# Performance work log

Measured on AMD Instinct MI355X. Metric: run time of the kernel, lower is better.

Reference implementation:

```python
import jax, jax.numpy as jnp
import numpy as np

N_NODES = 50000
N_EDGES = 800000
NUM_EMBS = 50000
EMB = 128
HID = 256
OUT = 128
NUM_GRAPHS = 256


def gcn_conv(x, W, b, src, dst, n):
    # PyG GCNConv: add self-loops, sym-normalize, aggregate, linear.
    h = x @ W  # [n, d_out]
    ones = jnp.ones((src.shape[0],), dtype=x.dtype)
    deg = jax.ops.segment_sum(ones, dst, num_segments=n) + 1.0  # +1 self-loop
    dinv = jax.lax.rsqrt(deg)  # deg^{-1/2}
    norm = dinv[src] * dinv[dst]  # per-edge norm
    msg = h[src] * norm[:, None]  # gather + scale  [E, d_out]
    agg = jax.ops.segment_sum(msg, dst, num_segments=n)
    agg = agg + h * (dinv * dinv)[:, None]  # self-loop term 1/deg[i]
    return agg + b


def scatter_mean(x, seg, num_segments):
    s = jax.ops.segment_sum(x, seg, num_segments=num_segments)
    cnt = jax.ops.segment_sum(jnp.ones((x.shape[0],), x.dtype), seg, num_segments=num_segments)
    return s / jnp.maximum(cnt, 1.0)[:, None]


def setup_inputs() -> dict:
    key = jax.random.key(0)
    ks = jax.random.split(key, 12)
    node_ids = jax.random.randint(ks[0], (N_NODES,), 0, NUM_EMBS)
    edge_index = jax.random.randint(ks[1], (2, N_EDGES), 0, N_NODES)
    batch = jnp.sort(jax.random.randint(ks[2], (N_NODES,), 0, NUM_GRAPHS))
    s = 0.05
    embed = jax.random.normal(ks[3], (NUM_EMBS, EMB), jnp.float32) * s
    W_in = jax.random.normal(ks[4], (EMB, HID), jnp.float32) * s
    b_in = jnp.zeros((HID,), jnp.float32)
    W_h1 = jax.random.normal(ks[5], (HID, HID), jnp.float32) * s
    b_h1 = jnp.zeros((HID,), jnp.float32)
    W_h2 = jax.random.normal(ks[6], (HID, HID), jnp.float32) * s
    b_h2 = jnp.zeros((HID,), jnp.float32)
    W_out = jax.random.normal(ks[7], (HID, OUT), jnp.float32) * s
    b_out = jnp.zeros((OUT,), jnp.float32)
    return {"node_ids": node_ids, "edge_index": edge_index, "batch": batch,
            "embed": embed, "W_in": W_in, "b_in": b_in,
            "W_h1": W_h1, "b_h1": b_h1, "W_h2": W_h2, "b_h2": b_h2,
            "W_out": W_out, "b_out": b_out}


def reference(node_ids, edge_index, batch, embed, W_in, b_in, W_h1, b_h1, W_h2, b_h2, W_out, b_out):
    src, dst = edge_index[0], edge_index[1]
    n = node_ids.shape[0]
    x = embed[node_ids]  # [N, EMB]
    x = gcn_conv(x, W_in, b_in, src, dst, n)
    x = jax.nn.relu(x)  # dropout = identity (eval mode)
    for W, b in ((W_h1, b_h1), (W_h2, b_h2)):
        x = gcn_conv(x, W, b, src, dst, n) + x  # residual
        x = jax.nn.relu(x)
    x = gcn_conv(x, W_out, b_out, src, dst, n)
    return scatter_mean(x, batch, NUM_GRAPHS)  # [NUM_GRAPHS, OUT]
```

## Files before the change

### kernel.cpp

```cpp
#include <hip/hip_runtime.h>
#include <hip/hip_bf16.h>
#include <hip/hip_fp8.h>

#define N_NODES 50000
#define N_EDGES 800000
#define EMB_D 128
#define HID_D 256
#define OUT_D 128
#define NGRAPH 256

#define SCAN_B ((N_NODES + 256) / 256)
#define MAX_CSR (N_EDGES + 7 * N_NODES)

typedef __attribute__((ext_vector_type(8))) short short8;
typedef __attribute__((ext_vector_type(4))) float floatx4;
typedef __attribute__((ext_vector_type(4))) unsigned short ushortx4;
typedef __attribute__((ext_vector_type(8))) unsigned short ushortx8;
typedef __attribute__((ext_vector_type(4))) unsigned char ucharx4;
typedef __attribute__((ext_vector_type(8))) unsigned char ucharx8;

__device__ inline unsigned short f2b(float f) {
    __hip_bfloat16 h = __float2bfloat16(f);
    return *reinterpret_cast<unsigned short*>(&h);
}

__device__ inline float b2f(unsigned short u) {
    union { unsigned int i; float f; } c;
    c.i = ((unsigned int)u) << 16;
    return c.f;
}

__device__ inline unsigned char f2f8(float f) {
    __hip_fp8_e4m3 v(f);
    return (unsigned char)v.__x;
}

__device__ inline float h2f(unsigned short u) { return b2f(u); }
__device__ inline float h2f(unsigned char u) {
    __hip_fp8_e4m3 v; v.__x = (__hip_fp8_storage_t)u;
    return (float)v;
}

template<int D, typename HT> struct HVec;
template<> struct HVec<128, unsigned short> { using T = ushortx4; };
template<> struct HVec<256, unsigned short> { using T = ushortx8; };
template<> struct HVec<128, unsigned char>  { using T = ucharx4;  };
template<> struct HVec<256, unsigned char>  { using T = ucharx8;  };

__global__ void rank_kernel(const int* __restrict__ dst, int* __restrict__ deg4,
                            int* __restrict__ pos) {
    int e = blockIdx.x * blockDim.x + threadIdx.x;
    if (e >= N_EDGES) return;
    pos[e] = atomicAdd(&deg4[(size_t)(e & 3) * N_NODES + dst[e]], 1);
}

__global__ void scan_a(const int* __restrict__ deg4, int* __restrict__ degt,
                       int* __restrict__ degp, int* __restrict__ sb4,
                       int* __restrict__ bsum, float* __restrict__ dinv) {
    __shared__ int red[256];
    int t = threadIdx.x;
    int i = blockIdx.x * 256 + t;
    int pad = 0;
    if (i < N_NODES) {
        int d0 = deg4[i];
        int d1 = deg4[(size_t)N_NODES + i];
        int d2 = deg4[(size_t)2 * N_NODES + i];
        int d3 = deg4[(size_t)3 * N_NODES + i];
        int tot = d0 + d1 + d2 + d3;
        degt[i] = tot;
        pad = (tot + 7) & ~7;
        degp[i] = pad;
        dinv[i] = rsqrtf((float)tot + 1.0f);
        sb4[i] = 0;
        sb4[(size_t)N_NODES + i] = d0;
        sb4[(size_t)2 * N_NODES + i] = d0 + d1;
        sb4[(size_t)3 * N_NODES + i] = d0 + d1 + d2;
    }
    red[t] = pad;
    __syncthreads();
    for (int off = 128; off > 0; off >>= 1) {
        if (t < off) red[t] += red[t + off];
        __syncthreads();
    }
    if (t == 0) bsum[blockIdx.x] = red[0];
}

__global__ void scan_b(const int* __restrict__ bsum, int* __restrict__ boff,
                       const int* __restrict__ batch, int* __restrict__ bstart) {
    int t = threadIdx.x;
    {
        int lo = 0, hi = N_NODES;
        while (lo < hi) {
            int mid = (lo + hi) >> 1;
            if (batch[mid] < t) lo = mid + 1;
            else hi = mid;
        }
        bstart[t] = lo;
        if (t == 0) bstart[NGRAPH] = N_NODES;
    }
    __shared__ int s[256];
    s[t] = (t < SCAN_B) ? bsum[t] : 0;
    __syncthreads();
    for (int off = 1; off < 256; off <<= 1) {
        int v = (t >= off) ? s[t - off] : 0;
        __syncthreads();
        s[t] += v;
        __syncthreads();
    }
    if (t < SCAN_B) boff[t] = (t == 0) ? 0 : s[t - 1];
}

__global__ void scan_c(const int* __restrict__ degp, const int* __restrict__ degt,
                       const int* __restrict__ boff, int* __restrict__ row_start,
                       unsigned int* __restrict__ csr) {
    __shared__ int s[256];
    int t = threadIdx.x;
    int i = blockIdx.x * 256 + t;
    int v = (i < N_NODES) ? degp[i] : 0;
    s[t] = v;
    __syncthreads();
    for (int off = 1; off < 256; off <<= 1) {
        int x = (t >= off) ? s[t - off] : 0;
        __syncthreads();
        s[t] += x;
        __syncthreads();
    }
    int excl = s[t] - v;
    int rs = boff[blockIdx.x] + excl;
    if (i <= N_NODES) row_start[i] = rs;
    if (i < N_NODES) {
        int e_true = rs + degt[i];
        int e_end  = rs + degp[i];
        for (int k = e_true; k < e_end; ++k) csr[k] = 0u;
    }
}

__global__ void scatter_kernel(const int* __restrict__ src, const int* __restrict__ dst,
                               const int* __restrict__ pos, const int* __restrict__ row_start,
                               const int* __restrict__ sb4, const float* __restrict__ dinv,
                               unsigned int* __restrict__ csr) {
    int e = blockIdx.x * blockDim.x + threadIdx.x;
    if (e >= N_EDGES) return;
    int s = src[e], d = dst[e];
    int slot = row_start[d] + sb4[(size_t)(e & 3) * N_NODES + d] + pos[e];
    csr[slot] = ((unsigned int)f2b(dinv[s] * dinv[d]) << 16) | (unsigned int)s;
}

template<int K, int D>
__device__ inline void wsplit_one(int idx, const float* __restrict__ W,
                                  short* __restrict__ wb) {
    int j = idx & 7;
    int l = (idx >> 3) & 63;
    int rest = idx >> 9;
    int kb = rest % (K / 32);
    int t = rest / (K / 32);
    int k = kb * 32 + (l >> 4) * 8 + j;
    int ncol = t * 16 + (l & 15);
    wb[idx] = (short)f2b(W[(size_t)k * D + ncol]);
}

__global__ void prep_kernel(const int* __restrict__ ids, const float* __restrict__ embed,
                            unsigned char* __restrict__ E8,
                            const float* __restrict__ W_in, const float* __restrict__ W_h1,
                            const float* __restrict__ W_h2, const float* __restrict__ W_out,
                            short* __restrict__ wb_in, short* __restrict__ wb_h1,
                            short* __restrict__ wb_h2, short* __restrict__ wb_out) {
    int idx = blockIdx.x * blockDim.x + threadIdx.x;
    constexpr int GV = N_NODES * (EMB_D / 4);
    if (idx < GV) {
        const int V = EMB_D / 4;
        int row = idx / V, c = idx % V;
        float4 v = ((const float4*)embed)[(size_t)ids[row] * V + c];
        ucharx4 u;
        u[0] = f2f8(v.x); u[1] = f2f8(v.y); u[2] = f2f8(v.z); u[3] = f2f8(v.w);
        ((ucharx4*)E8)[idx] = u;
        return;
    }
    int j = idx - GV;
    constexpr int S1 = EMB_D * HID_D;
    constexpr int S2 = S1 + HID_D * HID_D;
    constexpr int S3 = S2 + HID_D * HID_D;
    constexpr int S4 = S3 + HID_D * OUT_D;
    if (j < S1)      wsplit_one<EMB_D, HID_D>(j,      W_in,  wb_in);
    else if (j < S2) wsplit_one<HID_D, HID_D>(j - S1, W_h1,  wb_h1);
    else if (j < S3) wsplit_one<HID_D, HID_D>(j - S2, W_h2,  wb_h2);
    else if (j < S4) wsplit_one<HID_D, OUT_D>(j - S3, W_out, wb_out);
}

template<int D, typename HT, bool HASB, bool RES, bool RELU, bool BOUT>
__global__ __launch_bounds__(256) void agg_node(
        const int* __restrict__ row_start, const unsigned int* __restrict__ csr,
        const float* __restrict__ dinv, const HT* __restrict__ H,
        const float* __restrict__ b, float* __restrict__ OUTF,
        unsigned short* __restrict__ Pb) {
    constexpr int V2 = D / 32;
    using UV = typename HVec<D, HT>::T;
    using RV = typename HVec<D, unsigned short>::T;
    int wave = threadIdx.x >> 6, lane = threadIdx.x & 63;
    int i = blockIdx.x * 4 + wave;
    if (i >= N_NODES) return;
    int h = lane >> 5, q = lane & 31;
    const int off = q * V2;
    const HT* __restrict__ Hoff = H + off;
    float acc0[V2], acc1[V2];
#pragma unroll
    for (int v = 0; v < V2; ++v) { acc0[v] = 0.f; acc1[v] = 0.f; }
    int e0 = row_start[i], e1 = row_start[i + 1];
    if (e0 < e1) {
        unsigned int sn0 = csr[e0 + h];
        unsigned int sn1 = csr[e0 + 2 + h];
        unsigned int sn2 = csr[e0 + 4 + h];
        unsigned int sn3 = csr[e0 + 6 + h];
        int e = e0 + 8;
        for (;;) {
            UV u0 = *(const UV*)(Hoff + (size_t)(sn0 & 0xFFFFu) * D);
            UV u1 = *(const UV*)(Hoff + (size_t)(sn1 & 0xFFFFu) * D);
            UV u2 = *(const UV*)(Hoff + (size_t)(sn2 & 0xFFFFu) * D);
            UV u3 = *(const UV*)(Hoff + (size_t)(sn3 & 0xFFFFu) * D);
            float n0 = b2f((unsigned short)(sn0 >> 16));
            float n1 = b2f((unsigned short)(sn1 >> 16));
            float n2 = b2f((unsigned short)(sn2 >> 16));
            float n3 = b2f((unsigned short)(sn3 >> 16));
            bool more = (e < e1);
            unsigned int t0, t1, t2, t3;
            if (more) {
                t0 = csr[e + h];
                t1 = csr[e + 2 + h];
                t2 = csr[e + 4 + h];
                t3 = csr[e + 6 + h];
            }
#pragma unroll
            for (int v = 0; v < V2; ++v) acc0[v] = fmaf(h2f(u0[v]), n0, acc0[v]);
#pragma unroll
            for (int v = 0; v < V2; ++v) acc1[v] = fmaf(h2f(u1[v]), n1, acc1[v]);
#pragma unroll
            for (int v = 0; v < V2; ++v) acc0[v] = fmaf(h2f(u2[v]), n2, acc0[v]);
#pragma unroll
            for (int v = 0; v < V2; ++v) acc1[v] = fmaf(h2f(u3[v]), n3, acc1[v]);
            if (!more) break;
            sn0 = t0; sn1 = t1; sn2 = t2; sn3 = t3;
            e += 8;
        }
    }
#pragma unroll
    for (int v = 0; v < V2; ++v) {
        float s = acc0[v] + acc1[v];
        acc0[v] = s + __shfl_xor(s, 32);
    }
    if (h == 0) {
        float di = dinv[i];
        float d2 = di * di;
        UV us = *(const UV*)(Hoff + (size_t)i * D);
        RV rb;
        if (RES) rb = *(const RV*)(Pb + (size_t)i * D + off);
        RV ob;
#pragma unroll
        for (int v = 0; v < V2; ++v) {
            float val = acc0[v];
            val = fmaf(h2f(us[v]), d2, val);
            if (HASB) val += b[off + v];
            if (RES)  val += b2f(rb[v]);
            if (RELU) val = fmaxf(val, 0.f);
            if (BOUT) ob[v] = f2b(val);
            else      OUTF[(size_t)i * D + off + v] = val;
        }
        if (BOUT) *(RV*)(Pb + (size_t)i * D + off) = ob;
    }
}

template<int K, int D, bool BIAS, bool RELU, int OMODE>
__global__ __launch_bounds__(256) void gemm_mfma(
        const unsigned short* __restrict__ A_g, const short* __restrict__ Wb,
        const float* __restrict__ b, void* __restrict__ OutB, int n) {
    constexpr int LDK = K + 8;
    constexpr int NT = D / 64;
    constexpr int KB = K / 32;
    __shared__ __align__(16) short Ab[64 * LDK];

    int row0 = blockIdx.x * 64;
    constexpr int NF8 = 64 * (K / 8);
    for (int idx = threadIdx.x; idx < NF8; idx += 256) {
        int r = idx / (K / 8), c8 = idx % (K / 8);
        ushortx8 vh = {0, 0, 0, 0, 0, 0, 0, 0};
        if (row0 + r < n)
            vh = *(const ushortx8*)(A_g + (size_t)(row0 + r) * K + c8 * 8);
        *(ushortx8*)&Ab[r * LDK + c8 * 8] = vh;
    }
    __syncthreads();

    int wave = threadIdx.x >> 6, lane = threadIdx.x & 63;
    int quad = lane >> 4, lane15 = lane & 15;

    floatx4 acc[4][NT];
#pragma unroll
    for (int mt = 0; mt < 4; ++mt)
#pragma unroll
        for (int nt = 0; nt < NT; ++nt)
            acc[mt][nt] = (floatx4){0.f, 0.f, 0.f, 0.f};

#pragma unroll
    for (int kb = 0; kb < KB; ++kb) {
        short8 ah[4];
#pragma unroll
        for (int mt = 0; mt < 4; ++mt) {
            int addr = (mt * 16 + lane15) * LDK + kb * 32 + quad * 8;
            ah[mt] = *(const short8*)&Ab[addr];
        }
        short8 bh[NT];
#pragma unroll
        for (int nt = 0; nt < NT; ++nt) {
            int t = wave * NT + nt;
            size_t fb = ((size_t)(t * KB + kb) * 64 + lane) * 8;
            bh[nt] = *(const short8*)&Wb[fb];
        }
#pragma unroll
        for (int mt = 0; mt < 4; ++mt)
#pragma unroll
            for (int nt = 0; nt < NT; ++nt)
                acc[mt][nt] = __builtin_amdgcn_mfma_f32_16x16x32_bf16(ah[mt], bh[nt], acc[mt][nt], 0, 0, 0);
    }

#pragma unroll
    for (int mt = 0; mt < 4; ++mt) {
#pragma unroll
        for (int nt = 0; nt < NT; ++nt) {
            int col = wave * (NT * 16) + nt * 16 + lane15;
            float bj = BIAS ? b[col] : 0.f;
#pragma unroll
            for (int reg = 0; reg < 4; ++reg) {
                int row = row0 + mt * 16 + quad * 4 + reg;
                if (row < n) {
                    float v = acc[mt][nt][reg] + bj;
                    if (RELU) v = fmaxf(v, 0.f);
                    if (OMODE == 2) ((unsigned char*)OutB)[(size_t)row * D + col] = f2f8(v);
                    else            ((unsigned short*)OutB)[(size_t)row * D + col] = f2b(v);
                }
            }
        }
    }
}

__global__ void graph_mean(const int* __restrict__ bstart, const float* __restrict__ X,
                           float* __restrict__ out) {
    int g = blockIdx.x;
    int r0 = bstart[g], r1 = bstart[g + 1];
    int col = threadIdx.x & 127, rr = threadIdx.x >> 7;
    float acc = 0.f;
    for (int r = r0 + rr; r < r1; r += 2)
        acc += X[(size_t)r * OUT_D + col];
    __shared__ float sh[128];
    if (rr == 1) sh[col] = acc;
    __syncthreads();
    if (rr == 0) {
        float tot = acc + sh[col];
        int c = r1 - r0;
        out[(size_t)g * OUT_D + col] = tot / (float)(c > 0 ? c : 1);
    }
}

extern "C" void kernel_launch(void* const* d_in, const int* in_sizes, int n_in,
                              void* d_out, int out_size, void* d_ws, size_t ws_size,
                              hipStream_t stream) {
    const int* node_ids = (const int*)d_in[0];
    const int* edge_index = (const int*)d_in[1];
    const int* batch = (const int*)d_in[2];
    const float* embed = (const float*)d_in[3];
    const float* W_in  = (const float*)d_in[4];
    const float* b_in  = (const float*)d_in[5];
    const float* W_h1  = (const float*)d_in[6];
    const float* b_h1  = (const float*)d_in[7];
    const float* W_h2  = (const float*)d_in[8];
    const float* b_h2  = (const float*)d_in[9];
    const float* W_out = (const float*)d_in[10];
    const float* b_out = (const float*)d_in[11];
    float* out = (float*)d_out;

    const int* src = edge_index;
    const int* dst = edge_index + N_EDGES;

    char* w = (char*)d_ws;
    size_t o = 0;
    auto alloc = [&](size_t bytes) -> void* {
        void* p = w + o;
        o = (o + bytes + 255) & ~(size_t)255;
        return p;
    };
    int*   deg4     = (int*)alloc((size_t)4 * N_NODES * sizeof(int));
    int*   sb4      = (int*)alloc((size_t)4 * N_NODES * sizeof(int));
    int*   degt     = (int*)alloc((size_t)N_NODES * sizeof(int));
    int*   degp     = (int*)alloc((size_t)N_NODES * sizeof(int));
    int*   pos      = (int*)alloc((size_t)N_EDGES * sizeof(int));
    float* dinv     = (float*)alloc((size_t)N_NODES * sizeof(float));
    int*   bstart   = (int*)alloc((size_t)(NGRAPH + 1) * sizeof(int));
    int*   row_start= (int*)alloc((size_t)(N_NODES + 1) * sizeof(int));
    int*   bsum     = (int*)alloc((size_t)SCAN_B * sizeof(int));
    int*   boff     = (int*)alloc((size_t)SCAN_B * sizeof(int));
    unsigned int* csr = (unsigned int*)alloc((size_t)MAX_CSR * sizeof(unsigned int));
    unsigned short* Xb  = (unsigned short*)alloc((size_t)N_NODES * HID_D * sizeof(short));
    unsigned char*  E8  = (unsigned char*)alloc((size_t)N_NODES * EMB_D);
    unsigned char*  H8  = (unsigned char*)alloc((size_t)N_NODES * HID_D);
    unsigned short* A1b = (unsigned short*)alloc((size_t)N_NODES * 128 * sizeof(short));
    float* A1       = (float*)alloc((size_t)N_NODES * 128 * sizeof(float));
    short* Wb_in    = (short*)alloc((size_t)EMB_D * HID_D * sizeof(short));
    short* Wb_h1    = (short*)alloc((size_t)HID_D * HID_D * sizeof(short));
    short* Wb_h2    = (short*)alloc((size_t)HID_D * HID_D * sizeof(short));
    short* Wb_out   = (short*)alloc((size_t)HID_D * OUT_D * sizeof(short));
    unsigned char* H8_4 = H8;
    (void)ws_size;

    hipMemsetAsync(deg4, 0, (size_t)4 * N_NODES * sizeof(int), stream);

    rank_kernel<<<(N_EDGES + 255) / 256, 256, 0, stream>>>(dst, deg4, pos);
    scan_a<<<SCAN_B, 256, 0, stream>>>(deg4, degt, degp, sb4, bsum, dinv);
    scan_b<<<1, 256, 0, stream>>>(bsum, boff, batch, bstart);
    scan_c<<<SCAN_B, 256, 0, stream>>>(degp, degt, boff, row_start, csr);
    scatter_kernel<<<(N_EDGES + 255) / 256, 256, 0, stream>>>(src, dst, pos, row_start,
                                                              sb4, dinv, csr);

    constexpr int GV = N_NODES * (EMB_D / 4);
    prep_kernel<<<(GV + 196608 + 255) / 256, 256, 0, stream>>>(
        node_ids, embed, E8, W_in, W_h1, W_h2, W_out, Wb_in, Wb_h1, Wb_h2, Wb_out);

    const int gemm_grid = (N_NODES + 63) / 64;
    const int agg_grid = (N_NODES + 3) / 4;

    agg_node<128, unsigned char, false, false, false, true><<<agg_grid, 256, 0, stream>>>(
        row_start, csr, dinv, E8, nullptr, nullptr, A1b);
    gemm_mfma<128, 256, true, true, 0><<<gemm_grid, 256, 0, stream>>>(
        A1b, Wb_in, b_in, Xb, N_NODES);

    gemm_mfma<256, 256, false, false, 2><<<gemm_grid, 256, 0, stream>>>(
        Xb, Wb_h1, nullptr, H8, N_NODES);
    agg_node<256, unsigned char, true, true, true, true><<<agg_grid, 256, 0, stream>>>(
        row_start, csr, dinv, H8, b_h1, nullptr, Xb);

    gemm_mfma<256, 256, false, false, 2><<<gemm_grid, 256, 0, stream>>>(
        Xb, Wb_h2, nullptr, H8, N_NODES);
    agg_node<256, unsigned char, true, true, true, true><<<agg_grid, 256, 0, stream>>>(
        row_start, csr, dinv, H8, b_h2, nullptr, Xb);

    gemm_mfma<256, 128, false, false, 2><<<gemm_grid, 256, 0, stream>>>(
        Xb, Wb_out, nullptr, H8_4, N_NODES);
    agg_node<128, unsigned char, true, false, false, false><<<agg_grid, 256, 0, stream>>>(
        row_start, csr, dinv, H8_4, b_out, A1, nullptr);

    graph_mean<<<NGRAPH, 256, 0, stream>>>(bstart, A1, out);
}
```

Before: 395.7 us.

## Widen aggregation gathers to 8-element vectors and store final layer in bf16

The node aggregation kernel now has each lane gather 8 contiguous features. For D=128 this splits the wave into four 16-lane edge groups instead of two, so four edges are in flight per gather slot instead of two. The partial sums are then reduced across groups with a shuffle tree. The final aggregation writes bf16 instead of fp32, and the graph-mean kernel reads packed bf16 pairs with four row streams, which halves output traffic. Wider loads should improve memory efficiency, at the cost of extra shuffles and reduced precision on the last layer's output.

```diff
diff --git a/kernel.cpp b/kernel.cpp
--- a/kernel.cpp
+++ b/kernel.cpp
@@ -41,11 +41,9 @@
     return (float)v;
 }
 
-template<int D, typename HT> struct HVec;
-template<> struct HVec<128, unsigned short> { using T = ushortx4; };
-template<> struct HVec<256, unsigned short> { using T = ushortx8; };
-template<> struct HVec<128, unsigned char>  { using T = ucharx4;  };
-template<> struct HVec<256, unsigned char>  { using T = ucharx8;  };
+template<typename HT> struct UV8;
+template<> struct UV8<unsigned short> { using T = ushortx8; };
+template<> struct UV8<unsigned char>  { using T = ucharx8;  };
 
 __global__ void rank_kernel(const int* __restrict__ dst, int* __restrict__ deg4,
                             int* __restrict__ pos) {
@@ -193,61 +191,60 @@
         const float* __restrict__ dinv, const HT* __restrict__ H,
         const float* __restrict__ b, float* __restrict__ OUTF,
         unsigned short* __restrict__ Pb) {
-    constexpr int V2 = D / 32;
-    using UV = typename HVec<D, HT>::T;
-    using RV = typename HVec<D, unsigned short>::T;
+    constexpr int LPE = (D == 128) ? 16 : 32;
+    constexpr int NG  = 64 / LPE;
+    constexpr int NP  = 8 / NG;
+    using UV = typename UV8<HT>::T;
+    using RV = ushortx8;
     int wave = threadIdx.x >> 6, lane = threadIdx.x & 63;
     int i = blockIdx.x * 4 + wave;
     if (i >= N_NODES) return;
-    int h = lane >> 5, q = lane & 31;
-    const int off = q * V2;
+    int grp = lane / LPE, gl = lane % LPE;
+    const int off = gl * 8;
     const HT* __restrict__ Hoff = H + off;
-    float acc0[V2], acc1[V2];
-#pragma unroll
-    for (int v = 0; v < V2; ++v) { acc0[v] = 0.f; acc1[v] = 0.f; }
+    float acc0[8], acc1[8];
+#pragma unroll
+    for (int v = 0; v < 8; ++v) { acc0[v] = 0.f; acc1[v] = 0.f; }
     int e0 = row_start[i], e1 = row_start[i + 1];
     if (e0 < e1) {
-        unsigned int sn0 = csr[e0 + h];
-        unsigned int sn1 = csr[e0 + 2 + h];
-        unsigned int sn2 = csr[e0 + 4 + h];
-        unsigned int sn3 = csr[e0 + 6 + h];
+        unsigned int sn[NP];
+#pragma unroll
+        for (int k = 0; k < NP; ++k) sn[k] = csr[e0 + k * NG + grp];
         int e = e0 + 8;
         for (;;) {
-            UV u0 = *(const UV*)(Hoff + (size_t)(sn0 & 0xFFFFu) * D);
-            UV u1 = *(const UV*)(Hoff + (size_t)(sn1 & 0xFFFFu) * D);
-            UV u2 = *(const UV*)(Hoff + (size_t)(sn2 & 0xFFFFu) * D);
-            UV u3 = *(const UV*)(Hoff + (size_t)(sn3 & 0xFFFFu) * D);
-            float n0 = b2f((unsigned short)(sn0 >> 16));
-            float n1 = b2f((unsigned short)(sn1 >> 16));
-            float n2 = b2f((unsigned short)(sn2 >> 16));
-            float n3 = b2f((unsigned short)(sn3 >> 16));
+            UV u[NP];
+            float nn[NP];
+#pragma unroll
+            for (int k = 0; k < NP; ++k) {
+                u[k] = *(const UV*)(Hoff + (size_t)(sn[k] & 0xFFFFu) * D);
+                nn[k] = b2f((unsigned short)(sn[k] >> 16));
+            }
             bool more = (e < e1);
-            unsigned int t0, t1, t2, t3;
+            unsigned int t[NP];
             if (more) {
-                t0 = csr[e + h];
-                t1 = csr[e + 2 + h];
-                t2 = csr[e + 4 + h];
-                t3 = csr[e + 6 + h];
+#pragma unroll
+                for (int k = 0; k < NP; ++k) t[k] = csr[e + k * NG + grp];
             }
 #pragma unroll
-            for (int v = 0; v < V2; ++v) acc0[v] = fmaf(h2f(u0[v]), n0, acc0[v]);
-#pragma unroll
-            for (int v = 0; v < V2; ++v) acc1[v] = fmaf(h2f(u1[v]), n1, acc1[v]);
-#pragma unroll
-            for (int v = 0; v < V2; ++v) acc0[v] = fmaf(h2f(u2[v]), n2, acc0[v]);
-#pragma unroll
-            for (int v = 0; v < V2; ++v) acc1[v] = fmaf(h2f(u3[v]), n3, acc1[v]);
+            for (int k = 0; k < NP; ++k) {
+                float* A = (k & 1) ? acc1 : acc0;
+#pragma unroll
+                for (int v = 0; v < 8; ++v) A[v] = fmaf(h2f(u[k][v]), nn[k], A[v]);
+            }
             if (!more) break;
-            sn0 = t0; sn1 = t1; sn2 = t2; sn3 = t3;
+#pragma unroll
+            for (int k = 0; k < NP; ++k) sn[k] = t[k];
             e += 8;
         }
     }
 #pragma unroll
-    for (int v = 0; v < V2; ++v) {
+    for (int v = 0; v < 8; ++v) {
         float s = acc0[v] + acc1[v];
-        acc0[v] = s + __shfl_xor(s, 32);
-    }
-    if (h == 0) {
+#pragma unroll
+        for (int m = LPE; m < 64; m <<= 1) s += __shfl_xor(s, m);
+        acc0[v] = s;
+    }
+    if (grp == 0) {
         float di = dinv[i];
         float d2 = di * di;
         UV us = *(const UV*)(Hoff + (size_t)i * D);
@@ -255,7 +252,7 @@
         if (RES) rb = *(const RV*)(Pb + (size_t)i * D + off);
         RV ob;
 #pragma unroll
-        for (int v = 0; v < V2; ++v) {
+        for (int v = 0; v < 8; ++v) {
             float val = acc0[v];
             val = fmaf(h2f(us[v]), d2, val);
             if (HASB) val += b[off + v];
@@ -340,21 +337,27 @@
     }
 }
 
-__global__ void graph_mean(const int* __restrict__ bstart, const float* __restrict__ X,
+__global__ void graph_mean(const int* __restrict__ bstart, const unsigned short* __restrict__ X,
                            float* __restrict__ out) {
     int g = blockIdx.x;
     int r0 = bstart[g], r1 = bstart[g + 1];
-    int col = threadIdx.x & 127, rr = threadIdx.x >> 7;
-    float acc = 0.f;
-    for (int r = r0 + rr; r < r1; r += 2)
-        acc += X[(size_t)r * OUT_D + col];
-    __shared__ float sh[128];
-    if (rr == 1) sh[col] = acc;
+    int cp = threadIdx.x & 63, rr = threadIdx.x >> 6;
+    float a0 = 0.f, a1 = 0.f;
+    for (int r = r0 + rr; r < r1; r += 4) {
+        unsigned int w = ((const unsigned int*)X)[(size_t)r * 64 + cp];
+        a0 += b2f((unsigned short)(w & 0xFFFFu));
+        a1 += b2f((unsigned short)(w >> 16));
+    }
+    __shared__ float sh[2][3][64];
+    if (rr > 0) { sh[0][rr - 1][cp] = a0; sh[1][rr - 1][cp] = a1; }
     __syncthreads();
     if (rr == 0) {
-        float tot = acc + sh[col];
+        float t0 = a0 + sh[0][0][cp] + sh[0][1][cp] + sh[0][2][cp];
+        float t1 = a1 + sh[1][0][cp] + sh[1][1][cp] + sh[1][2][cp];
         int c = r1 - r0;
-        out[(size_t)g * OUT_D + col] = tot / (float)(c > 0 ? c : 1);
+        float inv = 1.f / (float)(c > 0 ? c : 1);
+        out[(size_t)g * OUT_D + cp * 2]     = t0 * inv;
+        out[(size_t)g * OUT_D + cp * 2 + 1] = t1 * inv;
     }
 }
 
@@ -400,7 +403,6 @@
     unsigned char*  E8  = (unsigned char*)alloc((size_t)N_NODES * EMB_D);
     unsigned char*  H8  = (unsigned char*)alloc((size_t)N_NODES * HID_D);
     unsigned short* A1b = (unsigned short*)alloc((size_t)N_NODES * 128 * sizeof(short));
-    float* A1       = (float*)alloc((size_t)N_NODES * 128 * sizeof(float));
     short* Wb_in    = (short*)alloc((size_t)EMB_D * HID_D * sizeof(short));
     short* Wb_h1    = (short*)alloc((size_t)HID_D * HID_D * sizeof(short));
     short* Wb_h2    = (short*)alloc((size_t)HID_D * HID_D * sizeof(short));
@@ -441,8 +443,8 @@
 
     gemm_mfma<256, 128, false, false, 2><<<gemm_grid, 256, 0, stream>>>(
         Xb, Wb_out, nullptr, H8_4, N_NODES);
-    agg_node<128, unsigned char, true, false, false, false><<<agg_grid, 256, 0, stream>>>(
-        row_start, csr, dinv, H8_4, b_out, A1, nullptr);
-
-    graph_mean<<<NGRAPH, 256, 0, stream>>>(bstart, A1, out);
-}
+    agg_node<128, unsigned char, true, false, false, true><<<agg_grid, 256, 0, stream>>>(
+        row_start, csr, dinv, H8_4, b_out, nullptr, A1b);
+
+    graph_mean<<<NGRAPH, 256, 0, stream>>>(bstart, A1b, out);
+}
```

After: 380.7 us. 3.8% less time.
